# Performance work log

Hardware: AMD Instinct MI355X
Metric: run time of the kernel (lower is better)

The kernel has to match this reference:

```python
import jax, jax.numpy as jnp
import numpy as np

B, S, H, NH, MRP = 4, 1024, 1024, 16, 64
DK = H // NH
VOCAB = 2 * MRP + 1


def setup_inputs() -> dict:
    key = jax.random.key(0)
    ks = jax.random.split(key, 12)
    sc = 1.0 / np.sqrt(H)
    inp = {
        "x": jax.random.normal(ks[0], (B, S, H), jnp.float32),
        "mask": jnp.ones((B, S), jnp.int32),
        "Wq": jax.random.normal(ks[1], (H, H), jnp.float32) * sc,
        "bq": jnp.zeros((H,), jnp.float32),
        "Wk": jax.random.normal(ks[2], (H, H), jnp.float32) * sc,
        "bk": jnp.zeros((H,), jnp.float32),
        "Wv": jax.random.normal(ks[3], (H, H), jnp.float32) * sc,
        "bv": jnp.zeros((H,), jnp.float32),
        "Wo": jax.random.normal(ks[4], (H, H), jnp.float32) * sc,
        "bo": jnp.zeros((H,), jnp.float32),
        "embK": jax.random.normal(ks[5], (VOCAB, DK), jnp.float32),
        "embV": jax.random.normal(ks[6], (VOCAB, DK), jnp.float32),
    }
    return inp


def _rel_idx(seq_len):
    r = jnp.arange(seq_len)
    dist = r[None, :] - r[:, None]              # (S, S)
    return jnp.clip(dist, -MRP, MRP) + MRP      # in [0, 2*MRP]


def reference(x, mask, Wq, bq, Wk, bk, Wv, bv, Wo, bo, embK, embV):
    # mask is dead in the original module (masked_softmax called w/o mask)
    nb, seq_len, _ = x.shape
    idx = _rel_idx(seq_len)
    rk = embK[idx]                              # (S, S, DK)
    rv = embV[idx]                              # (S, S, DK)

    def proj(W, b):
        return (x @ W.T + b).reshape(nb, seq_len, NH, DK).transpose(0, 2, 1, 3)

    q = proj(Wq, bq)                            # (B, NH, S, DK)
    k = proj(Wk, bk)
    v = proj(Wv, bv)

    # logits = QK^T + Q . R_k   (NOTE: no 1/sqrt(d_k) scaling in original)
    logits = jnp.einsum("bhqd,bhkd->bhqk", q, k) \
           + jnp.einsum("bhqd,qkd->bhqk", q, rk)
    w = jax.nn.softmax(logits, axis=-1)

    out = jnp.einsum("bhqk,bhkd->bhqd", w, v) \
        + jnp.einsum("bhqk,qkd->bhqd", w, rv)
    out = out.transpose(0, 2, 1, 3).reshape(nb, seq_len, NH * DK)
    return out @ Wo.T + bo
```

## Files before the change

kernel.cpp:

```cpp
#include <hip/hip_runtime.h>
#include <math.h>


#define TPB 256
#define TPA 512
constexpr int Bc = 4, Sc = 1024, Hc = 1024, NHc = 16, DKc = 64;
constexpr int NRc = 129;
constexpr float L2E = 1.44269504088896340736f;

using bf16x8 = __attribute__((ext_vector_type(8))) short;
using f32x4v = __attribute__((ext_vector_type(4))) float;

__device__ inline unsigned short f2bf(float f) {
  unsigned int u = __float_as_uint(f);
  return (unsigned short)((u + 0x7FFFu + ((u >> 16) & 1u)) >> 16);
}
__device__ inline float bf2f(unsigned short h) {
  return __uint_as_float(((unsigned int)h) << 16);
}

__global__ __launch_bounds__(TPB) void gemm_mfma3(
    const float* __restrict__ A, const float* __restrict__ W,
    const float* __restrict__ bias, float* __restrict__ C,
    int M, int N, int Kd) {
  __shared__ unsigned short Ah[128 * 32], Al[128 * 32];
  __shared__ unsigned short Bh[64 * 32],  Bl[64 * 32];

  const int tid = threadIdx.x;
  const int lane = tid & 63, wid = tid >> 6;
  const int wr = wid >> 1, wc = wid & 1;
  const int m0 = blockIdx.y * 128, n0 = blockIdx.x * 64;
  const int fr = lane & 15, fg = lane >> 4;

  const int ar = tid >> 1, akb = (tid & 1) * 16;
  const int br = tid >> 2, bkb = (tid & 3) * 8;
  const float* Ap = A + (size_t)(m0 + ar) * Kd + akb;
  const float* Bp = W + (size_t)(n0 + br) * Kd + bkb;

  f32x4v acc[4][2];
#pragma unroll
  for (int i = 0; i < 4; ++i)
#pragma unroll
    for (int j = 0; j < 2; ++j) acc[i][j] = (f32x4v)(0.f);

  float4 ra[4], rb[2];
#pragma unroll
  for (int q = 0; q < 4; ++q) ra[q] = *(const float4*)(Ap + q * 4);
#pragma unroll
  for (int q = 0; q < 2; ++q) rb[q] = *(const float4*)(Bp + q * 4);

  const int nK = Kd / 32;
  for (int kt = 0; kt < nK; ++kt) {
    __syncthreads();
#pragma unroll
    for (int q = 0; q < 2; ++q) {
      bf16x8 vh, vl;
#pragma unroll
      for (int e = 0; e < 8; ++e) {
        float v = ((const float*)ra)[q * 8 + e];
        unsigned short h = f2bf(v);
        vh[e] = (short)h;
        vl[e] = (short)f2bf(v - bf2f(h));
      }
      *(bf16x8*)(&Ah[ar * 32 + akb + q * 8]) = vh;
      *(bf16x8*)(&Al[ar * 32 + akb + q * 8]) = vl;
    }
    {
      bf16x8 vh, vl;
#pragma unroll
      for (int e = 0; e < 8; ++e) {
        float v = ((const float*)rb)[e];
        unsigned short h = f2bf(v);
        vh[e] = (short)h;
        vl[e] = (short)f2bf(v - bf2f(h));
      }
      *(bf16x8*)(&Bh[br * 32 + bkb]) = vh;
      *(bf16x8*)(&Bl[br * 32 + bkb]) = vl;
    }
    __syncthreads();
    if (kt + 1 < nK) {
      const float* Ap2 = Ap + (kt + 1) * 32;
      const float* Bp2 = Bp + (kt + 1) * 32;
#pragma unroll
      for (int q = 0; q < 4; ++q) ra[q] = *(const float4*)(Ap2 + q * 4);
#pragma unroll
      for (int q = 0; q < 2; ++q) rb[q] = *(const float4*)(Bp2 + q * 4);
    }
    bf16x8 fah[4], fal[4], fbh[2], fbl[2];
#pragma unroll
    for (int mf = 0; mf < 4; ++mf) {
      int r = wr * 64 + mf * 16 + fr;
      fah[mf] = *(const bf16x8*)(&Ah[r * 32 + fg * 8]);
      fal[mf] = *(const bf16x8*)(&Al[r * 32 + fg * 8]);
    }
#pragma unroll
    for (int nf = 0; nf < 2; ++nf) {
      int r = wc * 32 + nf * 16 + fr;
      fbh[nf] = *(const bf16x8*)(&Bh[r * 32 + fg * 8]);
      fbl[nf] = *(const bf16x8*)(&Bl[r * 32 + fg * 8]);
    }
#pragma unroll
    for (int mf = 0; mf < 4; ++mf)
#pragma unroll
      for (int nf = 0; nf < 2; ++nf) {
        acc[mf][nf] = __builtin_amdgcn_mfma_f32_16x16x32_bf16(
            fal[mf], fbh[nf], acc[mf][nf], 0, 0, 0);
        acc[mf][nf] = __builtin_amdgcn_mfma_f32_16x16x32_bf16(
            fah[mf], fbl[nf], acc[mf][nf], 0, 0, 0);
        acc[mf][nf] = __builtin_amdgcn_mfma_f32_16x16x32_bf16(
            fah[mf], fbh[nf], acc[mf][nf], 0, 0, 0);
      }
  }
#pragma unroll
  for (int nf = 0; nf < 2; ++nf) {
    int col = n0 + wc * 32 + nf * 16 + fr;
    float bv = bias[col];
#pragma unroll
    for (int mf = 0; mf < 4; ++mf)
#pragma unroll
      for (int rg = 0; rg < 4; ++rg) {
        int row = m0 + wr * 64 + mf * 16 + fg * 4 + rg;
        C[(size_t)row * N + col] = acc[mf][nf][rg] + bv;
      }
  }
}

__device__ __forceinline__ void stage_kv(
    int k0s, int pt, const float* Kp, const float* Vp,
    unsigned short* KH, unsigned short* KL,
    unsigned short* VH, unsigned short* VL) {
  const int r = pt & 63, c = pt >> 6;
  const float* ksrc = Kp + (size_t)(k0s + r) * Hc + c * 16;
  float kv[16];
#pragma unroll
  for (int q = 0; q < 4; ++q) {
    float4 t4 = *(const float4*)(ksrc + q * 4);
    kv[q * 4 + 0] = t4.x; kv[q * 4 + 1] = t4.y;
    kv[q * 4 + 2] = t4.z; kv[q * 4 + 3] = t4.w;
  }
  float vv[16];
  const float* vsrc = Vp + (size_t)(k0s + c * 16) * Hc + r;
#pragma unroll
  for (int j = 0; j < 16; ++j) vv[j] = vsrc[(size_t)j * Hc];
  bf16x8 kh[2], kl[2], vh[2], vl[2];
#pragma unroll
  for (int h2 = 0; h2 < 2; ++h2)
#pragma unroll
    for (int e = 0; e < 8; ++e) {
      const float a = kv[h2 * 8 + e];
      const unsigned short ha = f2bf(a);
      kh[h2][e] = (short)ha; kl[h2][e] = (short)f2bf(a - bf2f(ha));
      const float b = vv[h2 * 8 + e];
      const unsigned short hb = f2bf(b);
      vh[h2][e] = (short)hb; vl[h2][e] = (short)f2bf(b - bf2f(hb));
    }
  const int s0 = ((2 * c) ^ (r & 7)) * 8, s1 = ((2 * c + 1) ^ (r & 7)) * 8;
  *(bf16x8*)(KH + r * 64 + s0) = kh[0];
  *(bf16x8*)(KH + r * 64 + s1) = kh[1];
  *(bf16x8*)(KL + r * 64 + s0) = kl[0];
  *(bf16x8*)(KL + r * 64 + s1) = kl[1];
  *(bf16x8*)(VH + r * 64 + s0) = vh[0];
  *(bf16x8*)(VH + r * 64 + s1) = vh[1];
  *(bf16x8*)(VL + r * 64 + s0) = vl[0];
  *(bf16x8*)(VL + r * 64 + s1) = vl[1];
}

__global__ __launch_bounds__(TPA, 2) void attn_pc(
    const float* __restrict__ Q, const float* __restrict__ K,
    const float* __restrict__ V, const float* __restrict__ eK,
    const float* __restrict__ eV, float* __restrict__ O) {
  __shared__ __align__(16) unsigned char smem[141824];
  unsigned short* KsH = (unsigned short*)(smem);
  unsigned short* KsL = (unsigned short*)(smem + 16384);
  unsigned short* VtH = (unsigned short*)(smem + 32768);
  unsigned short* VtL = (unsigned short*)(smem + 49152);
  unsigned short* PsH = (unsigned short*)(smem + 65536);
  float* qr    = (float*)(smem + 74752);
  float* ws    = (float*)(smem + 107776);
  float* mhist = (float*)(smem + 140800);
  float* mfin  = (float*)(smem + 141568);

  const int tid = threadIdx.x;
  const int lane = tid & 63, w = tid >> 6;
  const int fr = lane & 15, g = lane >> 4;
  const bool consumer = (w < 4);
  const int qt = blockIdx.x, q0 = qt << 6;
  const int bb = (int)blockIdx.y >> 4, hh = (int)blockIdx.y & 15;
  const size_t base = ((size_t)bb * Sc) * Hc + (size_t)hh * DKc;
  const float* Qp = Q + base;
  const float* Kp = K + base;
  const float* Vp = V + base;

  float* Qs = ws;
  {
    const int row = tid >> 3, c0 = (tid & 7) * 8;
    const float* src = Qp + (size_t)(q0 + row) * Hc + c0;
    *(float4*)(Qs + row * 68 + c0)     = *(const float4*)(src);
    *(float4*)(Qs + row * 68 + c0 + 4) = *(const float4*)(src + 4);
  }
  if (tid < 192) mhist[tid] = -INFINITY;
  __syncthreads();
  for (int e = tid; e < 64 * NRc; e += TPA) {
    const int row = e / NRc, rr = e - row * NRc;
    const float* qv = Qs + row * 68;
    const float* ev = eK + rr * 64;
    float a = 0.f;
#pragma unroll
    for (int c = 0; c < 16; ++c) {
      float4 x = *(const float4*)(qv + c * 4);
      float4 y = *(const float4*)(ev + c * 4);
      a += x.x * y.x + x.y * y.y + x.z * y.z + x.w * y.w;
    }
    qr[e] = a;
  }
  __syncthreads();

  bf16x8 qh[2], ql[2];
  float qr0r[4], qr128r[4], m_[4], l_[4], pLo[4], pHi[4];
  f32x4v accO[4];
  if (consumer) {
#pragma unroll
    for (int ks = 0; ks < 2; ++ks) {
      const float* qsrc = Qp + (size_t)(q0 + w * 16 + fr) * Hc + ks * 32 + g * 8;
      float4 x0 = *(const float4*)(qsrc);
      float4 x1 = *(const float4*)(qsrc + 4);
      float xv[8] = {x0.x, x0.y, x0.z, x0.w, x1.x, x1.y, x1.z, x1.w};
#pragma unroll
      for (int e = 0; e < 8; ++e) {
        const unsigned short hb = f2bf(xv[e]);
        qh[ks][e] = (short)hb;
        ql[ks][e] = (short)f2bf(xv[e] - bf2f(hb));
      }
    }
#pragma unroll
    for (int r = 0; r < 4; ++r) {
      qr0r[r]   = qr[(w * 16 + g * 4 + r) * NRc + 0];
      qr128r[r] = qr[(w * 16 + g * 4 + r) * NRc + 128];
      m_[r] = -INFINITY; l_[r] = 0.f; pLo[r] = 0.f; pHi[r] = 0.f;
    }
#pragma unroll
    for (int dt = 0; dt < 4; ++dt) accO[dt] = (f32x4v)(0.f);
    for (int e = tid; e < 64 * NRc; e += TPB) ws[e] = 0.0f;
  } else {
    stage_kv(0, tid - 256, Kp, Vp, KsH, KsL, VtH, VtL);
  }
  __syncthreads();

  for (int kt = 0; kt < Sc / 64; ++kt) {
    const int k0 = kt << 6;
    const int band = kt - qt;
    const bool inband = (band >= -1) && (band <= 1);
    const int buf = kt & 1;
    if (consumer) {
      const unsigned short* KH = KsH + buf * 4096;
      const unsigned short* KL = KsL + buf * 4096;
      const unsigned short* VH = VtH + buf * 4096;
      const unsigned short* VL = VtL + buf * 4096;
      f32x4v sacc[4];
      __builtin_amdgcn_s_setprio(1);
#pragma unroll
      for (int t = 0; t < 4; ++t) {
        sacc[t] = (f32x4v)(0.f);
        const int kr = t * 16 + fr;
#pragma unroll
        for (int ks = 0; ks < 2; ++ks) {
          const int off = kr * 64 + (((ks * 4 + g) ^ (fr & 7)) * 8);
          bf16x8 kh = *(const bf16x8*)(KH + off);
          bf16x8 kl = *(const bf16x8*)(KL + off);
          sacc[t] = __builtin_amdgcn_mfma_f32_16x16x32_bf16(ql[ks], kh, sacc[t], 0, 0, 0);
          sacc[t] = __builtin_amdgcn_mfma_f32_16x16x32_bf16(qh[ks], kl, sacc[t], 0, 0, 0);
          sacc[t] = __builtin_amdgcn_mfma_f32_16x16x32_bf16(qh[ks], kh, sacc[t], 0, 0, 0);
        }
      }
      __builtin_amdgcn_s_setprio(0);
      if (inband) {
#pragma unroll
        for (int r = 0; r < 4; ++r) {
          const int prow = w * 16 + g * 4 + r;
#pragma unroll
          for (int t = 0; t < 4; ++t) {
            const int dd = (k0 + t * 16 + fr) - (q0 + prow);
            const int bk = dd < -64 ? 0 : (dd > 64 ? 128 : dd + 64);
            sacc[t][r] += qr[prow * NRc + bk];
          }
        }
      } else {
        const bool neg = band < 0;
#pragma unroll
        for (int r = 0; r < 4; ++r) {
          const float qc = neg ? qr0r[r] : qr128r[r];
#pragma unroll
          for (int t = 0; t < 4; ++t) sacc[t][r] += qc;
        }
      }
#pragma unroll
      for (int r = 0; r < 4; ++r) {
        float tm = fmaxf(fmaxf(sacc[0][r], sacc[1][r]), fmaxf(sacc[2][r], sacc[3][r]));
        tm = fmaxf(tm, __shfl_xor(tm, 1));
        tm = fmaxf(tm, __shfl_xor(tm, 2));
        tm = fmaxf(tm, __shfl_xor(tm, 4));
        tm = fmaxf(tm, __shfl_xor(tm, 8));
        const float mn = fmaxf(m_[r], tm);
        const float f = exp2f((m_[r] - mn) * L2E);
        m_[r] = mn;
        float p[4], psum = 0.f;
#pragma unroll
        for (int t = 0; t < 4; ++t) {
          p[t] = exp2f((sacc[t][r] - mn) * L2E);
          psum += p[t];
        }
        l_[r] = l_[r] * f + psum;
        pLo[r] *= f;
        pHi[r] *= f;
#pragma unroll
        for (int dt = 0; dt < 4; ++dt) accO[dt][r] *= f;
        const int prow = w * 16 + g * 4 + r;
        if (inband) {
#pragma unroll
          for (int t = 0; t < 4; ++t) {
            const int dd = (k0 + t * 16 + fr) - (q0 + prow);
            if (dd <= -64) pLo[r] += p[t];
            else if (dd >= 64) pHi[r] += p[t];
            else ws[prow * NRc + dd + 64] = p[t];
          }
          if (fr == 0) mhist[(band + 1) * 64 + prow] = mn;
        } else if (band < 0) {
          pLo[r] += psum;
        } else {
          pHi[r] += psum;
        }
#pragma unroll
        for (int t = 0; t < 4; ++t)
          PsH[w * 1152 + (g * 4 + r) * 72 + t * 16 + fr] = f2bf(p[t]);
      }
      asm volatile("s_waitcnt lgkmcnt(0)" ::: "memory");
      __builtin_amdgcn_sched_barrier(0);
      bf16x8 pah[2];
#pragma unroll
      for (int ks = 0; ks < 2; ++ks)
        pah[ks] = *(const bf16x8*)(PsH + w * 1152 + fr * 72 + ks * 32 + g * 8);
      __builtin_amdgcn_s_setprio(1);
#pragma unroll
      for (int dt = 0; dt < 4; ++dt) {
        const int vr = dt * 16 + fr;
#pragma unroll
        for (int ks = 0; ks < 2; ++ks) {
          const int off = vr * 64 + (((ks * 4 + g) ^ (fr & 7)) * 8);
          bf16x8 vh = *(const bf16x8*)(VH + off);
          bf16x8 vl = *(const bf16x8*)(VL + off);
          accO[dt] = __builtin_amdgcn_mfma_f32_16x16x32_bf16(pah[ks], vh, accO[dt], 0, 0, 0);
          accO[dt] = __builtin_amdgcn_mfma_f32_16x16x32_bf16(pah[ks], vl, accO[dt], 0, 0, 0);
        }
      }
      __builtin_amdgcn_s_setprio(0);
    } else {
      if (kt + 1 < Sc / 64) {
        const int nb = (kt + 1) & 1;
        stage_kv((kt + 1) << 6, tid - 256, Kp, Vp,
                 KsH + nb * 4096, KsL + nb * 4096,
                 VtH + nb * 4096, VtL + nb * 4096);
      }
    }
    __syncthreads();
  }

  if (consumer) {
    if (fr == 0) {
#pragma unroll
      for (int r = 0; r < 4; ++r) mfin[w * 16 + g * 4 + r] = m_[r];
    }
#pragma unroll
    for (int r = 0; r < 4; ++r) {
      l_[r] += __shfl_xor(l_[r], 1);  l_[r] += __shfl_xor(l_[r], 2);
      l_[r] += __shfl_xor(l_[r], 4);  l_[r] += __shfl_xor(l_[r], 8);
      pLo[r] += __shfl_xor(pLo[r], 1); pLo[r] += __shfl_xor(pLo[r], 2);
      pLo[r] += __shfl_xor(pLo[r], 4); pLo[r] += __shfl_xor(pLo[r], 8);
      pHi[r] += __shfl_xor(pHi[r], 1); pHi[r] += __shfl_xor(pHi[r], 2);
      pHi[r] += __shfl_xor(pHi[r], 4); pHi[r] += __shfl_xor(pHi[r], 8);
    }
  }
  __syncthreads();
  for (int e = tid; e < 64 * NRc; e += TPA) {
    const int row = e / NRc, b = e - row * NRc;
    const int kg = q0 + row + b - 64;
    if ((unsigned)kg < (unsigned)Sc) {
      const int lbt = (kg >> 6) - qt + 1;
      if ((unsigned)lbt < 3u)
        ws[e] *= exp2f((mhist[lbt * 64 + row] - mfin[row]) * L2E);
    }
  }
  __syncthreads();
  if (consumer && fr == 0) {
#pragma unroll
    for (int r = 0; r < 4; ++r) {
      const int prow = w * 16 + g * 4 + r;
      ws[prow * NRc + 0]   += pLo[r];
      ws[prow * NRc + 128] += pHi[r];
    }
  }
  float* eVs = (float*)smem;
  for (int e = tid; e < NRc * 16; e += TPA) {
    const int row = e >> 4, c4 = (e & 15) << 2;
    *(float4*)(eVs + row * 64 + c4) = *(const float4*)(eV + row * 64 + c4);
  }
  __syncthreads();
  if (consumer) {
    for (int r = 0; r < NRc; ++r) {
      float wsv[4], ev[4];
#pragma unroll
      for (int i = 0; i < 4; ++i) wsv[i] = ws[(w * 16 + g * 4 + i) * NRc + r];
#pragma unroll
      for (int dt = 0; dt < 4; ++dt) ev[dt] = eVs[r * 64 + dt * 16 + fr];
#pragma unroll
      for (int dt = 0; dt < 4; ++dt)
#pragma unroll
        for (int i = 0; i < 4; ++i)
          accO[dt][i] += wsv[i] * ev[dt];
    }
    float* Op = O + base;
#pragma unroll
    for (int r = 0; r < 4; ++r) {
      const float inv = 1.0f / l_[r];
      const int prow = w * 16 + g * 4 + r;
#pragma unroll
      for (int dt = 0; dt < 4; ++dt)
        Op[(size_t)(q0 + prow) * Hc + dt * 16 + fr] = accO[dt][r] * inv;
    }
  }
}

extern "C" void kernel_launch(void* const* d_in, const int* in_sizes, int n_in,
                              void* d_out, int out_size, void* d_ws, size_t ws_size,
                              hipStream_t stream) {
  const float* x    = (const float*)d_in[0];
  const float* Wq   = (const float*)d_in[2];
  const float* bq   = (const float*)d_in[3];
  const float* Wk   = (const float*)d_in[4];
  const float* bk   = (const float*)d_in[5];
  const float* Wv   = (const float*)d_in[6];
  const float* bv   = (const float*)d_in[7];
  const float* Wo   = (const float*)d_in[8];
  const float* bo   = (const float*)d_in[9];
  const float* embK = (const float*)d_in[10];
  const float* embV = (const float*)d_in[11];
  float* out = (float*)d_out;

  const size_t MxH = (size_t)Bc * Sc * Hc;
  float* Qb = (float*)d_ws;
  float* Kb = Qb + MxH;
  float* Vb = Kb + MxH;
  float* Ab = Vb + MxH;

  dim3 gg(Hc / 64, (Bc * Sc) / 128);
  gemm_mfma3<<<gg, TPB, 0, stream>>>(x, Wq, bq, Qb, Bc * Sc, Hc, Hc);
  gemm_mfma3<<<gg, TPB, 0, stream>>>(x, Wk, bk, Kb, Bc * Sc, Hc, Hc);
  gemm_mfma3<<<gg, TPB, 0, stream>>>(x, Wv, bv, Vb, Bc * Sc, Hc, Hc);

  dim3 ga(Sc / 64, Bc * NHc);
  attn_pc<<<ga, TPA, 0, stream>>>(Qb, Kb, Vb, embK, embV, Ab);

  dim3 go(Hc / 64, (Bc * Sc) / 128);
  gemm_mfma3<<<go, TPB, 0, stream>>>(Ab, Wo, bo, out, Bc * Sc, Hc, Hc);
}
```

Baseline: 697.8 us.

## Emit split-bf16 K and transposed V from projection GEMMs for attention staging

The K and V projection GEMMs now write hi/lo bf16 split outputs directly, with V stored transposed per head (d-major). The attention producer warps become simple swizzled 16-byte copies into LDS, one warp per buffer, replacing strided fp32 loads plus per-tile conversion. Each attention block no longer repeats the conversion, and the strided column reads of V go away. The cost is extra GEMM epilogue work and uncoalesced 8-byte transposed stores for V. f2bf also switches to the HIP intrinsic.

```diff
diff --git a/kernel.cpp b/kernel.cpp
--- a/kernel.cpp
+++ b/kernel.cpp
@@ -1,4 +1,5 @@
 #include <hip/hip_runtime.h>
+#include <hip/hip_bf16.h>
 #include <math.h>
 
 
@@ -12,16 +13,18 @@
 using f32x4v = __attribute__((ext_vector_type(4))) float;
 
 __device__ inline unsigned short f2bf(float f) {
-  unsigned int u = __float_as_uint(f);
-  return (unsigned short)((u + 0x7FFFu + ((u >> 16) & 1u)) >> 16);
+  __hip_bfloat16 h = __float2bfloat16(f);
+  return *reinterpret_cast<unsigned short*>(&h);
 }
 __device__ inline float bf2f(unsigned short h) {
   return __uint_as_float(((unsigned int)h) << 16);
 }
 
+template <int MODE>
 __global__ __launch_bounds__(TPB) void gemm_mfma3(
     const float* __restrict__ A, const float* __restrict__ W,
     const float* __restrict__ bias, float* __restrict__ C,
+    unsigned short* __restrict__ CH, unsigned short* __restrict__ CL,
     int M, int N, int Kd) {
   __shared__ unsigned short Ah[128 * 32], Al[128 * 32];
   __shared__ unsigned short Bh[64 * 32],  Bl[64 * 32];
@@ -113,62 +116,68 @@
   }
 #pragma unroll
   for (int nf = 0; nf < 2; ++nf) {
-    int col = n0 + wc * 32 + nf * 16 + fr;
-    float bv = bias[col];
-#pragma unroll
-    for (int mf = 0; mf < 4; ++mf)
-#pragma unroll
-      for (int rg = 0; rg < 4; ++rg) {
-        int row = m0 + wr * 64 + mf * 16 + fg * 4 + rg;
-        C[(size_t)row * N + col] = acc[mf][nf][rg] + bv;
-      }
-  }
-}
-
-__device__ __forceinline__ void stage_kv(
-    int k0s, int pt, const float* Kp, const float* Vp,
-    unsigned short* KH, unsigned short* KL,
-    unsigned short* VH, unsigned short* VL) {
-  const int r = pt & 63, c = pt >> 6;
-  const float* ksrc = Kp + (size_t)(k0s + r) * Hc + c * 16;
-  float kv[16];
-#pragma unroll
-  for (int q = 0; q < 4; ++q) {
-    float4 t4 = *(const float4*)(ksrc + q * 4);
-    kv[q * 4 + 0] = t4.x; kv[q * 4 + 1] = t4.y;
-    kv[q * 4 + 2] = t4.z; kv[q * 4 + 3] = t4.w;
-  }
-  float vv[16];
-  const float* vsrc = Vp + (size_t)(k0s + c * 16) * Hc + r;
-#pragma unroll
-  for (int j = 0; j < 16; ++j) vv[j] = vsrc[(size_t)j * Hc];
-  bf16x8 kh[2], kl[2], vh[2], vl[2];
-#pragma unroll
-  for (int h2 = 0; h2 < 2; ++h2)
-#pragma unroll
-    for (int e = 0; e < 8; ++e) {
-      const float a = kv[h2 * 8 + e];
-      const unsigned short ha = f2bf(a);
-      kh[h2][e] = (short)ha; kl[h2][e] = (short)f2bf(a - bf2f(ha));
-      const float b = vv[h2 * 8 + e];
-      const unsigned short hb = f2bf(b);
-      vh[h2][e] = (short)hb; vl[h2][e] = (short)f2bf(b - bf2f(hb));
-    }
-  const int s0 = ((2 * c) ^ (r & 7)) * 8, s1 = ((2 * c + 1) ^ (r & 7)) * 8;
-  *(bf16x8*)(KH + r * 64 + s0) = kh[0];
-  *(bf16x8*)(KH + r * 64 + s1) = kh[1];
-  *(bf16x8*)(KL + r * 64 + s0) = kl[0];
-  *(bf16x8*)(KL + r * 64 + s1) = kl[1];
-  *(bf16x8*)(VH + r * 64 + s0) = vh[0];
-  *(bf16x8*)(VH + r * 64 + s1) = vh[1];
-  *(bf16x8*)(VL + r * 64 + s0) = vl[0];
-  *(bf16x8*)(VL + r * 64 + s1) = vl[1];
+    const int col = n0 + wc * 32 + nf * 16 + fr;
+    const float bv = bias[col];
+#pragma unroll
+    for (int mf = 0; mf < 4; ++mf) {
+      const int row0 = m0 + wr * 64 + mf * 16 + fg * 4;
+      if (MODE == 0) {
+#pragma unroll
+        for (int rg = 0; rg < 4; ++rg)
+          C[(size_t)(row0 + rg) * N + col] = acc[mf][nf][rg] + bv;
+      } else if (MODE == 1) {
+#pragma unroll
+        for (int rg = 0; rg < 4; ++rg) {
+          const float v = acc[mf][nf][rg] + bv;
+          const unsigned short h = f2bf(v);
+          CH[(size_t)(row0 + rg) * N + col] = h;
+          CL[(size_t)(row0 + rg) * N + col] = f2bf(v - bf2f(h));
+        }
+      } else {
+        const int bb2 = row0 >> 10, s0 = row0 & 1023;
+        const int hh2 = col >> 6, d = col & 63;
+        const size_t basei =
+            (((size_t)bb2 * NHc + hh2) * DKc + d) * (size_t)Sc + s0;
+        unsigned short hs[4], ls[4];
+#pragma unroll
+        for (int rg = 0; rg < 4; ++rg) {
+          const float v = acc[mf][nf][rg] + bv;
+          hs[rg] = f2bf(v);
+          ls[rg] = f2bf(v - bf2f(hs[rg]));
+        }
+        uint2 ph, pl;
+        ph.x = (unsigned)hs[0] | ((unsigned)hs[1] << 16);
+        ph.y = (unsigned)hs[2] | ((unsigned)hs[3] << 16);
+        pl.x = (unsigned)ls[0] | ((unsigned)ls[1] << 16);
+        pl.y = (unsigned)ls[2] | ((unsigned)ls[3] << 16);
+        *(uint2*)(CH + basei) = ph;
+        *(uint2*)(CL + basei) = pl;
+      }
+    }
+  }
+}
+
+__device__ __forceinline__ void stage8(const unsigned short* __restrict__ g,
+                                       int lane, unsigned short* ldsT,
+                                       size_t koff) {
+  float4 t[8];
+#pragma unroll
+  for (int i = 0; i < 8; ++i) {
+    const int row = i * 8 + (lane >> 3);
+    const int gcol = (lane & 7) ^ (row & 7);
+    t[i] = *(const float4*)(g + koff + (size_t)row * 1024 + gcol * 8);
+  }
+#pragma unroll
+  for (int i = 0; i < 8; ++i)
+    *(float4*)(ldsT + (size_t)(i * 64 + lane) * 8) = t[i];
 }
 
 __global__ __launch_bounds__(TPA, 2) void attn_pc(
-    const float* __restrict__ Q, const float* __restrict__ K,
-    const float* __restrict__ V, const float* __restrict__ eK,
-    const float* __restrict__ eV, float* __restrict__ O) {
+    const float* __restrict__ Q,
+    const unsigned short* __restrict__ KHg, const unsigned short* __restrict__ KLg,
+    const unsigned short* __restrict__ VHg, const unsigned short* __restrict__ VLg,
+    const float* __restrict__ eK, const float* __restrict__ eV,
+    float* __restrict__ O) {
   __shared__ __align__(16) unsigned char smem[141824];
   unsigned short* KsH = (unsigned short*)(smem);
   unsigned short* KsL = (unsigned short*)(smem + 16384);
@@ -188,8 +197,6 @@
   const int bb = (int)blockIdx.y >> 4, hh = (int)blockIdx.y & 15;
   const size_t base = ((size_t)bb * Sc) * Hc + (size_t)hh * DKc;
   const float* Qp = Q + base;
-  const float* Kp = K + base;
-  const float* Vp = V + base;
 
   float* Qs = ws;
   {
@@ -218,6 +225,9 @@
   bf16x8 qh[2], ql[2];
   float qr0r[4], qr128r[4], m_[4], l_[4], pLo[4], pHi[4];
   f32x4v accO[4];
+  const unsigned short* gsrcT = nullptr;
+  unsigned short* ldsT = nullptr;
+  size_t kmul = 0;
   if (consumer) {
 #pragma unroll
     for (int ks = 0; ks < 2; ++ks) {
@@ -242,7 +252,14 @@
     for (int dt = 0; dt < 4; ++dt) accO[dt] = (f32x4v)(0.f);
     for (int e = tid; e < 64 * NRc; e += TPB) ws[e] = 0.0f;
   } else {
-    stage_kv(0, tid - 256, Kp, Vp, KsH, KsL, VtH, VtL);
+    const int wp = w - 4;
+    const size_t kb = (size_t)bb * Sc * Hc + (size_t)hh * DKc;
+    const size_t vb = ((size_t)(bb * NHc + hh)) * DKc * Sc;
+    if (wp == 0)      { gsrcT = KHg + kb; ldsT = KsH; kmul = 1024; }
+    else if (wp == 1) { gsrcT = KLg + kb; ldsT = KsL; kmul = 1024; }
+    else if (wp == 2) { gsrcT = VHg + vb; ldsT = VtH; kmul = 1; }
+    else              { gsrcT = VLg + vb; ldsT = VtL; kmul = 1; }
+    stage8(gsrcT, lane, ldsT, 0);
   }
   __syncthreads();
 
@@ -356,9 +373,7 @@
     } else {
       if (kt + 1 < Sc / 64) {
         const int nb = (kt + 1) & 1;
-        stage_kv((kt + 1) << 6, tid - 256, Kp, Vp,
-                 KsH + nb * 4096, KsL + nb * 4096,
-                 VtH + nb * 4096, VtL + nb * 4096);
+        stage8(gsrcT, lane, ldsT + nb * 4096, (size_t)(kt + 1) * 64 * kmul);
       }
     }
     __syncthreads();
@@ -447,18 +462,23 @@
 
   const size_t MxH = (size_t)Bc * Sc * Hc;
   float* Qb = (float*)d_ws;
-  float* Kb = Qb + MxH;
-  float* Vb = Kb + MxH;
-  float* Ab = Vb + MxH;
+  unsigned short* KH = (unsigned short*)(Qb + MxH);
+  unsigned short* KL = KH + MxH;
+  unsigned short* VH = KL + MxH;
+  unsigned short* VL = VH + MxH;
+  float* Ab = (float*)(VL + MxH);
 
   dim3 gg(Hc / 64, (Bc * Sc) / 128);
-  gemm_mfma3<<<gg, TPB, 0, stream>>>(x, Wq, bq, Qb, Bc * Sc, Hc, Hc);
-  gemm_mfma3<<<gg, TPB, 0, stream>>>(x, Wk, bk, Kb, Bc * Sc, Hc, Hc);
-  gemm_mfma3<<<gg, TPB, 0, stream>>>(x, Wv, bv, Vb, Bc * Sc, Hc, Hc);
+  gemm_mfma3<0><<<gg, TPB, 0, stream>>>(x, Wq, bq, Qb, nullptr, nullptr,
+                                        Bc * Sc, Hc, Hc);
+  gemm_mfma3<1><<<gg, TPB, 0, stream>>>(x, Wk, bk, nullptr, KH, KL,
+                                        Bc * Sc, Hc, Hc);
+  gemm_mfma3<2><<<gg, TPB, 0, stream>>>(x, Wv, bv, nullptr, VH, VL,
+                                        Bc * Sc, Hc, Hc);
 
   dim3 ga(Sc / 64, Bc * NHc);
-  attn_pc<<<ga, TPA, 0, stream>>>(Qb, Kb, Vb, embK, embV, Ab);
-
-  dim3 go(Hc / 64, (Bc * Sc) / 128);
-  gemm_mfma3<<<go, TPB, 0, stream>>>(Ab, Wo, bo, out, Bc * Sc, Hc, Hc);
-}
+  attn_pc<<<ga, TPA, 0, stream>>>(Qb, KH, KL, VH, VL, embK, embV, Ab);
+
+  gemm_mfma3<0><<<gg, TPB, 0, stream>>>(Ab, Wo, bo, out, nullptr, nullptr,
+                                        Bc * Sc, Hc, Hc);
+}
```

After: 672.7 us. -3.6%, faster.
